# Performance work log

Hardware: AMD Instinct MI355X
Metric: run time of the kernel (lower is better)

The kernel has to match this reference:

```python
import jax, jax.numpy as jnp
import numpy as np

B, S, D, H, DFF = 2, 2048, 768, 12, 3072
DK = D // H
LN_EPS = 1e-5

def _row_norm(x):
    # L2-normalize along last dim (torch F.normalize semantics)
    n = jnp.sqrt(jnp.sum(x * x, axis=-1, keepdims=True))
    return x / jnp.maximum(n, 1e-12)

def _layer_norm(x, gamma, beta):
    mu = jnp.mean(x, axis=-1, keepdims=True)
    var = jnp.mean((x - mu) ** 2, axis=-1, keepdims=True)
    return (x - mu) * jax.lax.rsqrt(var + LN_EPS) * gamma + beta

def setup_inputs() -> dict:
    key = jax.random.key(0)
    ks = jax.random.split(key, 16)
    sd = 1.0 / np.sqrt(D)
    sf = 1.0 / np.sqrt(DFF)
    inp = {
        "x": jax.random.normal(ks[0], (B, S, D), jnp.float32),
        "Wq": jax.random.uniform(ks[1], (D, D), jnp.float32, -sd, sd),
        "bq": jnp.zeros((D,), jnp.float32),
        "Wk": jax.random.uniform(ks[2], (D, D), jnp.float32, -sd, sd),
        "bk": jnp.zeros((D,), jnp.float32),
        "Wv": jax.random.uniform(ks[3], (D, D), jnp.float32, -sd, sd),
        "bv": jnp.zeros((D,), jnp.float32),
        "Wo": jax.random.uniform(ks[4], (D, D), jnp.float32, -sd, sd),
        "bo": jnp.zeros((D,), jnp.float32),
        "W1": jax.random.uniform(ks[5], (D, DFF), jnp.float32, -sd, sd),
        "b1": jnp.zeros((DFF,), jnp.float32),
        "W2": jax.random.uniform(ks[6], (DFF, D), jnp.float32, -sf, sf),
        "b2": jnp.zeros((D,), jnp.float32),
        "gamma": jnp.ones((D,), jnp.float32),
        "beta": jnp.zeros((D,), jnp.float32),
    }
    return inp

def reference(x, Wq, bq, Wk, bk, Wv, bv, Wo, bo, W1, b1, W2, b2, gamma, beta):
    b, s = x.shape[0], x.shape[1]
    # QKV projections, split into heads: [B,H,S,DK]
    def heads(y):
        return y.reshape(b, s, H, DK).transpose(0, 2, 1, 3)
    Q = heads(x @ Wq + bq)
    K = heads(x @ Wk + bk)
    V = heads(x @ Wv + bv)
    Qn = _row_norm(Q)
    Kn = _row_norm(K)
    scores = jnp.einsum("bhqd,bhkd->bhqk", Qn, Kn)
    attn = scores * scores  # squared dot-product, no softmax
    out = jnp.einsum("bhqk,bhkd->bhqd", attn, V)
    out = out.transpose(0, 2, 1, 3).reshape(b, s, D)
    attn_out = out @ Wo + bo
    x = _layer_norm(x + attn_out, gamma, beta)
    # FFN with exact GELU
    h = jax.nn.gelu(x @ W1 + b1, approximate=False)
    ff = h @ W2 + b2
    x = _layer_norm(x + ff, gamma, beta)  # norm1 reused
    return x
```

## Files before the change

### kernel.cpp

```cpp
#include <hip/hip_runtime.h>
#include <math.h>

using bf16   = __bf16;
using bf16x8 = __attribute__((ext_vector_type(8))) __bf16;
using bf16x4 = __attribute__((ext_vector_type(4))) __bf16;
using f32x4  = __attribute__((ext_vector_type(4))) float;

constexpr int S_   = 2048;
constexpr int D_   = 768;
constexpr int DFF_ = 3072;
constexpr int M_   = 4096;
constexpr int BH_  = 24;

__device__ __forceinline__ f32x4 mfma16(bf16x8 a, bf16x8 b, f32x4 c) {
    return __builtin_amdgcn_mfma_f32_16x16x32_bf16(a, b, c, 0, 0, 0);
}

__device__ __forceinline__ void gload16(const bf16* g, bf16* l) {
    __builtin_amdgcn_global_load_lds(
        (const __attribute__((address_space(1))) void*)g,
        (__attribute__((address_space(3))) void*)l, 16, 0, 0);
}

template<int N> __device__ __forceinline__ void wait_vmcnt() {
    if constexpr (N == 0)      asm volatile("s_waitcnt vmcnt(0)" ::: "memory");
    else if constexpr (N == 4) asm volatile("s_waitcnt vmcnt(4)" ::: "memory");
    else if constexpr (N == 6) asm volatile("s_waitcnt vmcnt(6)" ::: "memory");
    else if constexpr (N == 8) asm volatile("s_waitcnt vmcnt(8)" ::: "memory");
    else static_assert(N == 0, "unsupported vmcnt");
}
__device__ __forceinline__ void wait_lgkm0() {
    asm volatile("s_waitcnt lgkmcnt(0)" ::: "memory");
}

__device__ __forceinline__ int xcd_swz(int orig, int nwg) {
    return (orig & 7) * (nwg >> 3) + (orig >> 3);
}

__device__ __forceinline__ float gelu_f(float v) {
    float y = 1.5957691f * (v + 0.044715f * v * v * v);
    return v / (1.0f + __expf(-y));
}

__global__ __launch_bounds__(256)
void pack_x_kernel(const float* __restrict__ x, bf16* __restrict__ xb) {
    const int i = blockIdx.x * 256 + threadIdx.x;
    float4 v = ((const float4*)x)[i];
    bf16x4 o;
    o[0] = (bf16)v.x; o[1] = (bf16)v.y; o[2] = (bf16)v.z; o[3] = (bf16)v.w;
    ((bf16x4*)xb)[i] = o;
}

__global__ __launch_bounds__(256)
void merge_ao_kernel(const bf16* __restrict__ a, const bf16* __restrict__ b,
                     bf16* __restrict__ o) {
    const long i = ((long)blockIdx.x * 256 + threadIdx.x) * 8;
    bf16x8 va = *(const bf16x8*)&a[i];
    bf16x8 vb = *(const bf16x8*)&b[i];
    bf16x8 vo;
#pragma unroll
    for (int j = 0; j < 8; j++) vo[j] = (bf16)((float)va[j] + (float)vb[j]);
    *(bf16x8*)&o[i] = vo;
}

__global__ __launch_bounds__(256)
void wt_all_kernel(const float* __restrict__ Wq, const float* __restrict__ Wk,
                   const float* __restrict__ Wv, const float* __restrict__ Wo,
                   const float* __restrict__ W1, const float* __restrict__ W2,
                   bf16* __restrict__ Wqkvt, bf16* __restrict__ Wot,
                   bf16* __restrict__ W1t, bf16* __restrict__ W2t) {
    int bid = blockIdx.x;
    const float* in; bf16* out; int K, N, t;
    if (bid < 576) {
        int m = bid / 144; t = bid % 144; K = 768; N = 768;
        in  = (m == 0) ? Wq : (m == 1) ? Wk : (m == 2) ? Wv : Wo;
        out = (m == 3) ? Wot : Wqkvt + (size_t)m * 768 * 768;
    } else if (bid < 1152) {
        t = bid - 576; K = 768; N = 3072; in = W1; out = W1t;
    } else {
        t = bid - 1152; K = 3072; N = 768; in = W2; out = W2t;
    }
    const int ntx = N / 64;
    const int n0 = (t % ntx) * 64, k0 = (t / ntx) * 64;

    __shared__ __align__(16) bf16 T[64][72];
    const int tt = threadIdx.x;
    const int r  = tt >> 2, c0 = (tt & 3) * 16;
    const float* src = in + (size_t)(k0 + r) * N + n0 + c0;
#pragma unroll
    for (int j = 0; j < 16; j += 4) {
        float4 v = *(const float4*)(src + j);
        T[r][c0 + j + 0] = (bf16)v.x;
        T[r][c0 + j + 1] = (bf16)v.y;
        T[r][c0 + j + 2] = (bf16)v.z;
        T[r][c0 + j + 3] = (bf16)v.w;
    }
    __syncthreads();
    bf16x8 o0, o1;
#pragma unroll
    for (int j = 0; j < 8; j++) { o0[j] = T[c0 + j][r]; o1[j] = T[c0 + 8 + j][r]; }
    bf16* dst = out + (size_t)(n0 + r) * K + k0 + c0;
    *(bf16x8*)(dst)     = o0;
    *(bf16x8*)(dst + 8) = o1;
}

template<int EPI, int K, int BM, int BN, int WR, int WC>
__global__ __launch_bounds__(256)
void gemm_bt(const bf16* __restrict__ A, const bf16* __restrict__ Bt,
             const float* __restrict__ bias0, const float* __restrict__ bias1,
             const float* __restrict__ bias2, const float* __restrict__ residf,
             const bf16* __restrict__ residb, bf16* __restrict__ outb,
             bf16* __restrict__ qo, bf16* __restrict__ ko, bf16* __restrict__ vo) {
    constexpr int MR  = BM / WR / 16;
    constexpr int NR  = BN / WC / 16;
    constexpr int GA  = BM / 32;
    constexpr int GB  = BN / 32;
    constexpr int NPT = GA + GB;
    constexpr int NCOL = (EPI == 0) ? 2304 : (EPI == 2) ? 3072 : 768;
    constexpr int NBX  = NCOL / BN;
    __shared__ __align__(16) bf16 Al[2 * BM * 64];
    __shared__ __align__(16) bf16 Bl[2 * BN * 64];
    const int tid  = threadIdx.x;
    const int lane = tid & 63, w = tid >> 6;
    const int wr = w / WC, wc = w % WC;
    const int wg = xcd_swz(blockIdx.x, gridDim.x);
    const int m0 = (wg / NBX) * BM, n0 = (wg % NBX) * BN;
    const int g = lane >> 4, q = lane & 15;
    const int srow = lane >> 3;
    const int schunk = (((lane & 7) ^ ((lane >> 3) & 7))) * 8;

    f32x4 acc[MR][NR] = {};

    const bf16* gaA = A  + (long)(m0 + w * (BM / 4) + srow) * K + schunk;
    const bf16* gaB = Bt + (long)(n0 + w * (BN / 4) + srow) * K + schunk;

    auto stage = [&](int buf, int kt) {
#pragma unroll
        for (int i = 0; i < GA; i++)
            gload16(gaA + kt + (long)i * 8 * K,
                    &Al[buf * BM * 64 + (w * (BM / 4) + i * 8) * 64]);
#pragma unroll
        for (int i = 0; i < GB; i++)
            gload16(gaB + kt + (long)i * 8 * K,
                    &Bl[buf * BN * 64 + (w * (BN / 4) + i * 8) * 64]);
    };
    auto compute = [&](int buf) {
#pragma unroll
        for (int c = 0; c < 2; c++) {
            const int rch = ((c * 4 + g) ^ (q & 7)) * 8;
            bf16x8 af[MR], bfr[NR];
#pragma unroll
            for (int i = 0; i < MR; i++)
                af[i] = *(const bf16x8*)
                    &Al[buf * BM * 64 + (wr * (BM / WR) + i * 16 + q) * 64 + rch];
#pragma unroll
            for (int i = 0; i < NR; i++)
                bfr[i] = *(const bf16x8*)
                    &Bl[buf * BN * 64 + (wc * (BN / WC) + i * 16 + q) * 64 + rch];
#pragma unroll
            for (int mi = 0; mi < MR; mi++)
#pragma unroll
                for (int ni = 0; ni < NR; ni++)
                    acc[mi][ni] = mfma16(af[mi], bfr[ni], acc[mi][ni]);
        }
    };

    stage(0, 0);
    stage(1, 64);
    int cur = 0;
    for (int kt = 0; kt < K - 64; kt += 64) {
        wait_vmcnt<NPT>();
        __builtin_amdgcn_s_barrier();
        compute(cur);
        wait_lgkm0();
        __builtin_amdgcn_s_barrier();
        if (kt + 128 < K) stage(cur, kt + 128);
        cur ^= 1;
    }
    wait_vmcnt<0>();
    __builtin_amdgcn_s_barrier();
    compute(cur);

#pragma unroll
    for (int mi = 0; mi < MR; mi++) {
        if (EPI == 0) {
            const int col0  = n0 + wc * 64;
            const int which = (col0 >= 1536) ? 2 : (col0 >= 768 ? 1 : 0);
            const int row0  = m0 + wr * (BM / WR) + mi * 16 + g * 4;
            float val[NR][4];
#pragma unroll
            for (int ni = 0; ni < NR; ni++) {
                const int dd = col0 + ni * 16 + q - which * 768;
                const float bias = (which == 0 ? bias0 : which == 1 ? bias1 : bias2)[dd];
#pragma unroll
                for (int r = 0; r < 4; r++) val[ni][r] = acc[mi][ni][r] + bias;
            }
            if (which <= 1) {
#pragma unroll
                for (int r = 0; r < 4; r++) {
                    float ss = val[0][r] * val[0][r];
#pragma unroll
                    for (int ni = 1; ni < NR; ni++) ss += val[ni][r] * val[ni][r];
                    ss += __shfl_xor(ss, 1);
                    ss += __shfl_xor(ss, 2);
                    ss += __shfl_xor(ss, 4);
                    ss += __shfl_xor(ss, 8);
                    const float rn = 1.0f / fmaxf(sqrtf(ss), 1e-12f);
#pragma unroll
                    for (int ni = 0; ni < NR; ni++) val[ni][r] *= rn;
                }
            }
            const int dd0 = col0 - which * 768;
            const int hh  = dd0 >> 6;
            const long bh = (long)(row0 >> 11) * 12 + hh;
#pragma unroll
            for (int ni = 0; ni < NR; ni++) {
                const int dk = ni * 16 + q;
                if (which == 2) {
                    bf16x4 pv;
#pragma unroll
                    for (int r = 0; r < 4; r++) pv[r] = (bf16)val[ni][r];
                    *(bf16x4*)&vo[(bh * 64 + dk) * 2048 + (row0 & 2047)] = pv;
                } else {
                    bf16* dst = (which == 0) ? qo : ko;
#pragma unroll
                    for (int r = 0; r < 4; r++)
                        dst[(bh * 2048 + ((row0 + r) & 2047)) * 64 + dk] = (bf16)val[ni][r];
                }
            }
        } else {
#pragma unroll
            for (int ni = 0; ni < NR; ni++) {
                const int col  = n0 + wc * (BN / WC) + ni * 16 + q;
                const int row0 = m0 + wr * (BM / WR) + mi * 16 + g * 4;
                const float bias = bias0[col];
                if (EPI == 1) {
#pragma unroll
                    for (int r = 0; r < 4; r++) {
                        const int row = row0 + r;
                        outb[(long)row * 768 + col] =
                            (bf16)(acc[mi][ni][r] + bias + residf[(long)row * 768 + col]);
                    }
                } else if (EPI == 3) {
#pragma unroll
                    for (int r = 0; r < 4; r++) {
                        const int row = row0 + r;
                        outb[(long)row * 768 + col] =
                            (bf16)(acc[mi][ni][r] + bias + (float)residb[(long)row * 768 + col]);
                    }
                } else {
#pragma unroll
                    for (int r = 0; r < 4; r++) {
                        const float v = acc[mi][ni][r] + bias;
                        outb[(long)(row0 + r) * 3072 + col] = (bf16)gelu_f(v);
                    }
                }
            }
        }
    }
}

__global__ __launch_bounds__(256, 3)
void attn_kernel(const bf16* __restrict__ Qn, const bf16* __restrict__ Kn,
                 const bf16* __restrict__ Vt, bf16* __restrict__ AOp) {
    const int wg  = xcd_swz(blockIdx.x, gridDim.x);
    const int bh  = wg >> 5;
    const int rem = wg & 31;
    const int kvhalf = rem >> 4;
    const int qblk   = rem & 15;
    const int tid = threadIdx.x, lane = tid & 63, w = tid >> 6;
    const int g = lane >> 4, q15 = lane & 15;
    const int qbase = qblk * 128 + w * 32;
    const int kv0   = kvhalf * 1024;
    constexpr int NT = 16;

    __shared__ __align__(16) bf16 Kl[2][64][72];
    __shared__ __align__(16) bf16 Vl[2][64][72];
    __shared__ __align__(16) bf16 Pl[4][16][72];
    bf16 (*Pw)[72] = Pl[w];

    const bf16* Qp = Qn + (long)bh * S_ * 64;
    const bf16* Kp = Kn + (long)bh * S_ * 64 + (long)kv0 * 64;
    const bf16* Vp = Vt + (long)bh * 64 * S_ + kv0;
    bf16* AOo = AOp + (long)kvhalf * M_ * D_;

    const int srow = tid >> 3, scol = (tid & 7) * 8;

    bf16x8 qf00 = *(const bf16x8*)&Qp[(long)(qbase + q15) * 64 + g * 8];
    bf16x8 qf01 = *(const bf16x8*)&Qp[(long)(qbase + q15) * 64 + 32 + g * 8];
    bf16x8 qf10 = *(const bf16x8*)&Qp[(long)(qbase + 16 + q15) * 64 + g * 8];
    bf16x8 qf11 = *(const bf16x8*)&Qp[(long)(qbase + 16 + q15) * 64 + 32 + g * 8];

    f32x4 o0[4] = {}, o1[4] = {};

    bf16x8 aK0, aK1, aV0, aV1, bK0, bK1, bV0, bV1;
    auto gloadA = [&](int kt) {
        aK0 = *(const bf16x8*)&Kp[(long)(kt + srow) * 64 + scol];
        aK1 = *(const bf16x8*)&Kp[(long)(kt + 32 + srow) * 64 + scol];
        aV0 = *(const bf16x8*)&Vp[(long)srow * S_ + kt + scol];
        aV1 = *(const bf16x8*)&Vp[(long)(32 + srow) * S_ + kt + scol];
    };
    auto gloadB = [&](int kt) {
        bK0 = *(const bf16x8*)&Kp[(long)(kt + srow) * 64 + scol];
        bK1 = *(const bf16x8*)&Kp[(long)(kt + 32 + srow) * 64 + scol];
        bV0 = *(const bf16x8*)&Vp[(long)srow * S_ + kt + scol];
        bV1 = *(const bf16x8*)&Vp[(long)(32 + srow) * S_ + kt + scol];
    };
    auto stageA = [&](int buf) {
        *(bf16x8*)&Kl[buf][srow][scol]      = aK0;
        *(bf16x8*)&Kl[buf][32 + srow][scol] = aK1;
        *(bf16x8*)&Vl[buf][srow][scol]      = aV0;
        *(bf16x8*)&Vl[buf][32 + srow][scol] = aV1;
    };
    auto stageB = [&](int buf) {
        *(bf16x8*)&Kl[buf][srow][scol]      = bK0;
        *(bf16x8*)&Kl[buf][32 + srow][scol] = bK1;
        *(bf16x8*)&Vl[buf][srow][scol]      = bV0;
        *(bf16x8*)&Vl[buf][32 + srow][scol] = bV1;
    };

    auto compute = [&](int cur) {
        bf16x8 kf[4][2];
#pragma unroll
        for (int ni = 0; ni < 4; ni++)
#pragma unroll
            for (int c = 0; c < 2; c++)
                kf[ni][c] = *(const bf16x8*)&Kl[cur][ni * 16 + q15][c * 32 + g * 8];
        f32x4 s0[4], s1[4];
#pragma unroll
        for (int ni = 0; ni < 4; ni++) {
            s0[ni] = mfma16(kf[ni][0], qf00, f32x4{0.f, 0.f, 0.f, 0.f});
            s0[ni] = mfma16(kf[ni][1], qf01, s0[ni]);
            s1[ni] = mfma16(kf[ni][0], qf10, f32x4{0.f, 0.f, 0.f, 0.f});
            s1[ni] = mfma16(kf[ni][1], qf11, s1[ni]);
        }
#pragma unroll
        for (int ni = 0; ni < 4; ni++) {
            bf16x4 p0;
#pragma unroll
            for (int r = 0; r < 4; r++) { float v = s0[ni][r]; p0[r] = (bf16)(v * v); }
            *(bf16x4*)&Pw[q15][ni * 16 + g * 4] = p0;
        }
        bf16x8 pf00 = *(const bf16x8*)&Pw[q15][g * 8];
        bf16x8 pf01 = *(const bf16x8*)&Pw[q15][32 + g * 8];
#pragma unroll
        for (int ni = 0; ni < 4; ni++) {
            bf16x4 p1;
#pragma unroll
            for (int r = 0; r < 4; r++) { float v = s1[ni][r]; p1[r] = (bf16)(v * v); }
            *(bf16x4*)&Pw[q15][ni * 16 + g * 4] = p1;
        }
        bf16x8 pf10 = *(const bf16x8*)&Pw[q15][g * 8];
        bf16x8 pf11 = *(const bf16x8*)&Pw[q15][32 + g * 8];
        bf16x8 vf[4][2];
#pragma unroll
        for (int ni = 0; ni < 4; ni++)
#pragma unroll
            for (int c = 0; c < 2; c++)
                vf[ni][c] = *(const bf16x8*)&Vl[cur][ni * 16 + q15][c * 32 + g * 8];
#pragma unroll
        for (int ni = 0; ni < 4; ni++) {
            o0[ni] = mfma16(pf00, vf[ni][0], o0[ni]);
            o0[ni] = mfma16(pf01, vf[ni][1], o0[ni]);
            o1[ni] = mfma16(pf10, vf[ni][0], o1[ni]);
            o1[ni] = mfma16(pf11, vf[ni][1], o1[ni]);
        }
    };

    gloadA(0);
    stageA(0);
    gloadB(64);
    __syncthreads();
    for (int t = 0; t <= NT - 4; t += 2) {
        stageB(1);
        gloadA((t + 2) * 64);
        compute(0);
        __syncthreads();
        stageA(0);
        if (t + 3 < NT) gloadB((t + 3) * 64);
        compute(1);
        __syncthreads();
    }
    stageB(1);
    compute(0);
    __syncthreads();
    compute(1);

    const int b = bh / 12, h = bh % 12;
#pragma unroll
    for (int ni = 0; ni < 4; ni++)
#pragma unroll
        for (int r = 0; r < 4; r++) {
            const int s0r = qbase + g * 4 + r;
            AOo[((long)b * S_ + s0r) * D_ + h * 64 + ni * 16 + q15] = (bf16)o0[ni][r];
            const int s1r = qbase + 16 + g * 4 + r;
            AOo[((long)b * S_ + s1r) * D_ + h * 64 + ni * 16 + q15] = (bf16)o1[ni][r];
        }
}

template<bool WB>
__global__ __launch_bounds__(256)
void ln_kernel(const bf16* __restrict__ y, const float* __restrict__ gamma,
               const float* __restrict__ beta, float* __restrict__ xo,
               bf16* __restrict__ xob) {
    __shared__ float sa[4], sb[4];
    const int row = blockIdx.x, t = threadIdx.x;
    const bf16* yr = y + (long)row * 768;
    float v0 = (float)yr[t], v1 = (float)yr[t + 256], v2 = (float)yr[t + 512];
    float s  = v0 + v1 + v2;
    float ss = v0 * v0 + v1 * v1 + v2 * v2;
#pragma unroll
    for (int o = 32; o; o >>= 1) { s += __shfl_xor(s, o); ss += __shfl_xor(ss, o); }
    if ((t & 63) == 0) { sa[t >> 6] = s; sb[t >> 6] = ss; }
    __syncthreads();
    s  = sa[0] + sa[1] + sa[2] + sa[3];
    ss = sb[0] + sb[1] + sb[2] + sb[3];
    const float mu   = s * (1.0f / 768.0f);
    const float var  = ss * (1.0f / 768.0f) - mu * mu;
    const float rstd = rsqrtf(var + 1e-5f);
#pragma unroll
    for (int i = 0; i < 3; i++) {
        const int c = t + i * 256;
        const float vv = (i == 0) ? v0 : (i == 1) ? v1 : v2;
        const float ov = (vv - mu) * rstd * gamma[c] + beta[c];
        if (WB) xob[(long)row * 768 + c] = (bf16)ov;
        else    xo[(long)row * 768 + c] = ov;
    }
}

extern "C" void kernel_launch(void* const* d_in, const int* in_sizes, int n_in,
                              void* d_out, int out_size, void* d_ws, size_t ws_size,
                              hipStream_t stream) {
    const float* x     = (const float*)d_in[0];
    const float* Wq    = (const float*)d_in[1];
    const float* bq    = (const float*)d_in[2];
    const float* Wk    = (const float*)d_in[3];
    const float* bk    = (const float*)d_in[4];
    const float* Wv    = (const float*)d_in[5];
    const float* bv    = (const float*)d_in[6];
    const float* Wo    = (const float*)d_in[7];
    const float* bo    = (const float*)d_in[8];
    const float* W1    = (const float*)d_in[9];
    const float* b1    = (const float*)d_in[10];
    const float* W2    = (const float*)d_in[11];
    const float* b2    = (const float*)d_in[12];
    const float* gamma = (const float*)d_in[13];
    const float* beta  = (const float*)d_in[14];

    char* p = (char*)d_ws;
    auto alloc = [&](size_t bytes) -> void* {
        void* r = p;
        p += (bytes + 255) & ~(size_t)255;
        return r;
    };
    bf16*  Xb    = (bf16*)alloc((size_t)M_ * D_ * 2);
    bf16*  Wqkvt = (bf16*)alloc((size_t)2304 * 768 * 2);
    bf16*  Wot   = (bf16*)alloc((size_t)768 * 768 * 2);
    bf16*  W1t   = (bf16*)alloc((size_t)3072 * 768 * 2);
    bf16*  W2t   = (bf16*)alloc((size_t)768 * 3072 * 2);
    bf16*  Qh    = (bf16*)alloc((size_t)BH_ * S_ * 64 * 2);
    bf16*  Kh    = (bf16*)alloc((size_t)BH_ * S_ * 64 * 2);
    bf16*  Vt    = (bf16*)alloc((size_t)BH_ * S_ * 64 * 2);
    bf16*  AOp   = (bf16*)alloc((size_t)2 * M_ * D_ * 2);
    bf16*  AO    = (bf16*)alloc((size_t)M_ * D_ * 2);
    bf16*  y1b   = (bf16*)alloc((size_t)M_ * D_ * 2);
    bf16*  x1b   = (bf16*)alloc((size_t)M_ * D_ * 2);
    bf16*  hbuf  = (bf16*)alloc((size_t)M_ * DFF_ * 2);
    bf16*  y2b   = y1b;

    pack_x_kernel<<<(M_ * D_) / 1024, 256, 0, stream>>>(x, Xb);
    wt_all_kernel<<<1728, 256, 0, stream>>>(Wq, Wk, Wv, Wo, W1, W2,
                                            Wqkvt, Wot, W1t, W2t);

    gemm_bt<0, 768, 64, 128, 2, 2><<<64 * 18, 256, 0, stream>>>(
        Xb, Wqkvt, bq, bk, bv, nullptr, nullptr, nullptr, Qh, Kh, Vt);

    attn_kernel<<<2 * 16 * BH_, 256, 0, stream>>>(Qh, Kh, Vt, AOp);
    merge_ao_kernel<<<(M_ * D_) / 2048, 256, 0, stream>>>(
        AOp, AOp + (size_t)M_ * D_, AO);

    gemm_bt<1, 768, 64, 64, 2, 2><<<12 * 64, 256, 0, stream>>>(
        AO, Wot, bo, nullptr, nullptr, x, nullptr, y1b, nullptr, nullptr, nullptr);
    ln_kernel<true><<<M_, 256, 0, stream>>>(y1b, gamma, beta, nullptr, x1b);

    gemm_bt<2, 768, 64, 128, 2, 2><<<64 * 24, 256, 0, stream>>>(
        x1b, W1t, b1, nullptr, nullptr, nullptr, nullptr, hbuf, nullptr, nullptr, nullptr);
    gemm_bt<3, 3072, 64, 64, 2, 2><<<12 * 64, 256, 0, stream>>>(
        hbuf, W2t, b2, nullptr, nullptr, nullptr, x1b, y2b, nullptr, nullptr, nullptr);
    ln_kernel<false><<<M_, 256, 0, stream>>>(y2b, gamma, beta, (float*)d_out, nullptr);
}
```

Measured before the change: 162.7 us.

## Split-K the Wo and W2 GEMMs with BN=128 and fuse partial merge into LayerNorm

The Wo and W2 projections (N=768) now use 64x128 tiles with a two-way split over K. Each half writes a bf16 partial result, and a new merge_ln kernel sums the partials, adds bias and residual, and applies LayerNorm. This removes the residual and bias epilogue from the GEMMs and drops the separate ln kernels. The aim is more reuse per tile while keeping the grid size up, at the cost of writing and re-reading bf16 partials and an extra rounding step before the sum.

```diff
diff --git a/kernel.cpp b/kernel.cpp
--- a/kernel.cpp
+++ b/kernel.cpp
@@ -61,6 +61,45 @@
 #pragma unroll
     for (int j = 0; j < 8; j++) vo[j] = (bf16)((float)va[j] + (float)vb[j]);
     *(bf16x8*)&o[i] = vo;
+}
+
+template<bool FIRST>
+__global__ __launch_bounds__(256)
+void merge_ln_kernel(const bf16* __restrict__ pp, const float* __restrict__ bias,
+                     const float* __restrict__ residf, const bf16* __restrict__ residb,
+                     const float* __restrict__ gamma, const float* __restrict__ beta,
+                     float* __restrict__ outf, bf16* __restrict__ outb) {
+    __shared__ float sa[4], sb[4];
+    const int row = blockIdx.x, t = threadIdx.x;
+    const bf16* p0 = pp + (long)row * 768;
+    const bf16* p1 = pp + (long)M_ * 768 + (long)row * 768;
+    float v[3];
+#pragma unroll
+    for (int i = 0; i < 3; i++) {
+        const int c = t + i * 256;
+        float y = (float)p0[c] + (float)p1[c] + bias[c];
+        if (FIRST) y += residf[(long)row * 768 + c];
+        else       y += (float)residb[(long)row * 768 + c];
+        v[i] = y;
+    }
+    float s  = v[0] + v[1] + v[2];
+    float ss = v[0] * v[0] + v[1] * v[1] + v[2] * v[2];
+#pragma unroll
+    for (int o = 32; o; o >>= 1) { s += __shfl_xor(s, o); ss += __shfl_xor(ss, o); }
+    if ((t & 63) == 0) { sa[t >> 6] = s; sb[t >> 6] = ss; }
+    __syncthreads();
+    s  = sa[0] + sa[1] + sa[2] + sa[3];
+    ss = sb[0] + sb[1] + sb[2] + sb[3];
+    const float mu   = s * (1.0f / 768.0f);
+    const float var  = ss * (1.0f / 768.0f) - mu * mu;
+    const float rstd = rsqrtf(var + 1e-5f);
+#pragma unroll
+    for (int i = 0; i < 3; i++) {
+        const int c = t + i * 256;
+        const float ov = (v[i] - mu) * rstd * gamma[c] + beta[c];
+        if (FIRST) outb[(long)row * 768 + c] = (bf16)ov;
+        else       outf[(long)row * 768 + c] = ov;
+    }
 }
 
 __global__ __launch_bounds__(256)
@@ -104,18 +143,19 @@
     *(bf16x8*)(dst + 8) = o1;
 }
 
-template<int EPI, int K, int BM, int BN, int WR, int WC>
+template<int EPI, int K, int BM, int BN, int WR, int WC, int KSPLIT>
 __global__ __launch_bounds__(256)
 void gemm_bt(const bf16* __restrict__ A, const bf16* __restrict__ Bt,
              const float* __restrict__ bias0, const float* __restrict__ bias1,
-             const float* __restrict__ bias2, const float* __restrict__ residf,
-             const bf16* __restrict__ residb, bf16* __restrict__ outb,
+             const float* __restrict__ bias2,
+             bf16* __restrict__ outb,
              bf16* __restrict__ qo, bf16* __restrict__ ko, bf16* __restrict__ vo) {
     constexpr int MR  = BM / WR / 16;
     constexpr int NR  = BN / WC / 16;
     constexpr int GA  = BM / 32;
     constexpr int GB  = BN / 32;
     constexpr int NPT = GA + GB;
+    constexpr int KS  = K / KSPLIT;
     constexpr int NCOL = (EPI == 0) ? 2304 : (EPI == 2) ? 3072 : 768;
     constexpr int NBX  = NCOL / BN;
     __shared__ __align__(16) bf16 Al[2 * BM * 64];
@@ -124,15 +164,18 @@
     const int lane = tid & 63, w = tid >> 6;
     const int wr = w / WC, wc = w % WC;
     const int wg = xcd_swz(blockIdx.x, gridDim.x);
-    const int m0 = (wg / NBX) * BM, n0 = (wg % NBX) * BN;
+    const int ks = wg % KSPLIT;
+    const int tt = wg / KSPLIT;
+    const int m0 = (tt / NBX) * BM, n0 = (tt % NBX) * BN;
+    const int kb = ks * KS;
     const int g = lane >> 4, q = lane & 15;
     const int srow = lane >> 3;
     const int schunk = (((lane & 7) ^ ((lane >> 3) & 7))) * 8;
 
     f32x4 acc[MR][NR] = {};
 
-    const bf16* gaA = A  + (long)(m0 + w * (BM / 4) + srow) * K + schunk;
-    const bf16* gaB = Bt + (long)(n0 + w * (BN / 4) + srow) * K + schunk;
+    const bf16* gaA = A  + (long)(m0 + w * (BM / 4) + srow) * K + kb + schunk;
+    const bf16* gaB = Bt + (long)(n0 + w * (BN / 4) + srow) * K + kb + schunk;
 
     auto stage = [&](int buf, int kt) {
 #pragma unroll
@@ -168,13 +211,13 @@
     stage(0, 0);
     stage(1, 64);
     int cur = 0;
-    for (int kt = 0; kt < K - 64; kt += 64) {
+    for (int kt = 0; kt < KS - 64; kt += 64) {
         wait_vmcnt<NPT>();
         __builtin_amdgcn_s_barrier();
         compute(cur);
         wait_lgkm0();
         __builtin_amdgcn_s_barrier();
-        if (kt + 128 < K) stage(cur, kt + 128);
+        if (kt + 128 < KS) stage(cur, kt + 128);
         cur ^= 1;
     }
     wait_vmcnt<0>();
@@ -228,33 +271,27 @@
                         dst[(bh * 2048 + ((row0 + r) & 2047)) * 64 + dk] = (bf16)val[ni][r];
                 }
             }
-        } else {
+        } else if (EPI == 2) {
 #pragma unroll
             for (int ni = 0; ni < NR; ni++) {
                 const int col  = n0 + wc * (BN / WC) + ni * 16 + q;
                 const int row0 = m0 + wr * (BM / WR) + mi * 16 + g * 4;
                 const float bias = bias0[col];
-                if (EPI == 1) {
-#pragma unroll
-                    for (int r = 0; r < 4; r++) {
-                        const int row = row0 + r;
-                        outb[(long)row * 768 + col] =
-                            (bf16)(acc[mi][ni][r] + bias + residf[(long)row * 768 + col]);
-                    }
-                } else if (EPI == 3) {
-#pragma unroll
-                    for (int r = 0; r < 4; r++) {
-                        const int row = row0 + r;
-                        outb[(long)row * 768 + col] =
-                            (bf16)(acc[mi][ni][r] + bias + (float)residb[(long)row * 768 + col]);
-                    }
-                } else {
-#pragma unroll
-                    for (int r = 0; r < 4; r++) {
-                        const float v = acc[mi][ni][r] + bias;
-                        outb[(long)(row0 + r) * 3072 + col] = (bf16)gelu_f(v);
-                    }
+#pragma unroll
+                for (int r = 0; r < 4; r++) {
+                    const float v = acc[mi][ni][r] + bias;
+                    outb[(long)(row0 + r) * 3072 + col] = (bf16)gelu_f(v);
                 }
+            }
+        } else {
+#pragma unroll
+            for (int ni = 0; ni < NR; ni++) {
+                const int col  = n0 + wc * (BN / WC) + ni * 16 + q;
+                const int row0 = m0 + wr * (BM / WR) + mi * 16 + g * 4;
+#pragma unroll
+                for (int r = 0; r < 4; r++)
+                    outb[(long)ks * M_ * 768 + (long)(row0 + r) * 768 + col] =
+                        (bf16)acc[mi][ni][r];
             }
         }
     }
@@ -396,36 +433,6 @@
             const int s1r = qbase + 16 + g * 4 + r;
             AOo[((long)b * S_ + s1r) * D_ + h * 64 + ni * 16 + q15] = (bf16)o1[ni][r];
         }
-}
-
-template<bool WB>
-__global__ __launch_bounds__(256)
-void ln_kernel(const bf16* __restrict__ y, const float* __restrict__ gamma,
-               const float* __restrict__ beta, float* __restrict__ xo,
-               bf16* __restrict__ xob) {
-    __shared__ float sa[4], sb[4];
-    const int row = blockIdx.x, t = threadIdx.x;
-    const bf16* yr = y + (long)row * 768;
-    float v0 = (float)yr[t], v1 = (float)yr[t + 256], v2 = (float)yr[t + 512];
-    float s  = v0 + v1 + v2;
-    float ss = v0 * v0 + v1 * v1 + v2 * v2;
-#pragma unroll
-    for (int o = 32; o; o >>= 1) { s += __shfl_xor(s, o); ss += __shfl_xor(ss, o); }
-    if ((t & 63) == 0) { sa[t >> 6] = s; sb[t >> 6] = ss; }
-    __syncthreads();
-    s  = sa[0] + sa[1] + sa[2] + sa[3];
-    ss = sb[0] + sb[1] + sb[2] + sb[3];
-    const float mu   = s * (1.0f / 768.0f);
-    const float var  = ss * (1.0f / 768.0f) - mu * mu;
-    const float rstd = rsqrtf(var + 1e-5f);
-#pragma unroll
-    for (int i = 0; i < 3; i++) {
-        const int c = t + i * 256;
-        const float vv = (i == 0) ? v0 : (i == 1) ? v1 : v2;
-        const float ov = (vv - mu) * rstd * gamma[c] + beta[c];
-        if (WB) xob[(long)row * 768 + c] = (bf16)ov;
-        else    xo[(long)row * 768 + c] = ov;
-    }
 }
 
 extern "C" void kernel_launch(void* const* d_in, const int* in_sizes, int n_in,
@@ -463,29 +470,31 @@
     bf16*  Vt    = (bf16*)alloc((size_t)BH_ * S_ * 64 * 2);
     bf16*  AOp   = (bf16*)alloc((size_t)2 * M_ * D_ * 2);
     bf16*  AO    = (bf16*)alloc((size_t)M_ * D_ * 2);
-    bf16*  y1b   = (bf16*)alloc((size_t)M_ * D_ * 2);
+    bf16*  pp    = (bf16*)alloc((size_t)2 * M_ * 768 * 2);
     bf16*  x1b   = (bf16*)alloc((size_t)M_ * D_ * 2);
     bf16*  hbuf  = (bf16*)alloc((size_t)M_ * DFF_ * 2);
-    bf16*  y2b   = y1b;
 
     pack_x_kernel<<<(M_ * D_) / 1024, 256, 0, stream>>>(x, Xb);
     wt_all_kernel<<<1728, 256, 0, stream>>>(Wq, Wk, Wv, Wo, W1, W2,
                                             Wqkvt, Wot, W1t, W2t);
 
-    gemm_bt<0, 768, 64, 128, 2, 2><<<64 * 18, 256, 0, stream>>>(
-        Xb, Wqkvt, bq, bk, bv, nullptr, nullptr, nullptr, Qh, Kh, Vt);
+    gemm_bt<0, 768, 64, 128, 2, 2, 1><<<64 * 18, 256, 0, stream>>>(
+        Xb, Wqkvt, bq, bk, bv, nullptr, Qh, Kh, Vt);
 
     attn_kernel<<<2 * 16 * BH_, 256, 0, stream>>>(Qh, Kh, Vt, AOp);
     merge_ao_kernel<<<(M_ * D_) / 2048, 256, 0, stream>>>(
         AOp, AOp + (size_t)M_ * D_, AO);
 
-    gemm_bt<1, 768, 64, 64, 2, 2><<<12 * 64, 256, 0, stream>>>(
-        AO, Wot, bo, nullptr, nullptr, x, nullptr, y1b, nullptr, nullptr, nullptr);
-    ln_kernel<true><<<M_, 256, 0, stream>>>(y1b, gamma, beta, nullptr, x1b);
-
-    gemm_bt<2, 768, 64, 128, 2, 2><<<64 * 24, 256, 0, stream>>>(
-        x1b, W1t, b1, nullptr, nullptr, nullptr, nullptr, hbuf, nullptr, nullptr, nullptr);
-    gemm_bt<3, 3072, 64, 64, 2, 2><<<12 * 64, 256, 0, stream>>>(
-        hbuf, W2t, b2, nullptr, nullptr, nullptr, x1b, y2b, nullptr, nullptr, nullptr);
-    ln_kernel<false><<<M_, 256, 0, stream>>>(y2b, gamma, beta, (float*)d_out, nullptr);
-}
+    gemm_bt<1, 768, 64, 128, 2, 2, 2><<<64 * 6 * 2, 256, 0, stream>>>(
+        AO, Wot, nullptr, nullptr, nullptr, pp, nullptr, nullptr, nullptr);
+    merge_ln_kernel<true><<<M_, 256, 0, stream>>>(
+        pp, bo, x, nullptr, gamma, beta, nullptr, x1b);
+
+    gemm_bt<2, 768, 64, 128, 2, 2, 1><<<64 * 24, 256, 0, stream>>>(
+        x1b, W1t, b1, nullptr, nullptr, hbuf, nullptr, nullptr, nullptr);
+
+    gemm_bt<3, 3072, 64, 128, 2, 2, 2><<<64 * 6 * 2, 256, 0, stream>>>(
+        hbuf, W2t, nullptr, nullptr, nullptr, pp, nullptr, nullptr, nullptr);
+    merge_ln_kernel<false><<<M_, 256, 0, stream>>>(
+        pp, b2, nullptr, x1b, gamma, beta, (float*)d_out, nullptr);
+}
```

Measured after the change: 156.3 us. -3.9%, faster.
